# Kernel optimization log

Hardware: AMD Instinct MI355X
Metric: run time of the kernel (lower is better)

The kernel has to match this reference:

```python
import jax, jax.numpy as jnp
import numpy as np

N_HEADS = 16

def setup_inputs() -> dict:
    key = jax.random.key(0)
    k1, k2, k3 = jax.random.split(key, 3)
    B, T, C = 2, 2048, 1024
    x = jax.random.normal(k1, (B, T, C), dtype=jnp.float32)
    W_qkv = jax.random.normal(k2, (3 * C, C), dtype=jnp.float32) * 0.02
    b_qkv = jnp.zeros((3 * C,), dtype=jnp.float32)
    W_proj = jax.random.normal(k3, (C, C), dtype=jnp.float32) * 0.02
    b_proj = jnp.zeros((C,), dtype=jnp.float32)
    return {"x": x, "W_qkv": W_qkv, "b_qkv": b_qkv, "W_proj": W_proj, "b_proj": b_proj}

def reference(x, W_qkv, b_qkv, W_proj, b_proj):
    B, T, C = x.shape
    H = N_HEADS
    hd = C // H
    # fused QKV projection: (B,T,3C)
    qkv = x @ W_qkv.T + b_qkv
    # mirror torch: reshape to (B,T,H,3*hd) then chunk along last dim
    qkv = qkv.reshape(B, T, H, 3 * hd)
    q, k, v = jnp.split(qkv, 3, axis=-1)  # each (B,T,H,hd)
    q = q / jnp.sqrt(jnp.asarray(hd, dtype=q.dtype))
    # scaled dot-product attention, non-causal, full matrix (faithful to source)
    att = jnp.einsum('bihd,bjhd->bhij', q, k)  # (B,H,T,T)
    att = jax.nn.softmax(att, axis=-1)
    out = jnp.einsum('bhij,bjhd->bihd', att, v)  # (B,T,H,hd)
    out = out.reshape(B, T, C)
    return out @ W_proj.T + b_proj
```

## Files before the change

### kernel.cpp

```cpp
#include <hip/hip_runtime.h>


typedef __bf16 bf16x4 __attribute__((ext_vector_type(4)));
typedef __bf16 bf16x8 __attribute__((ext_vector_type(8)));
typedef float  f32x4  __attribute__((ext_vector_type(4)));

#define AS1(p) ((const __attribute__((address_space(1))) void*)(p))
#define AS3(p) ((__attribute__((address_space(3))) void*)(p))

__global__ __launch_bounds__(256)
void cvt_all(const float* __restrict__ a, const float* __restrict__ b,
             const float* __restrict__ c, __bf16* __restrict__ oa,
             __bf16* __restrict__ ob, __bf16* __restrict__ oc,
             int na, int nb, int nc)
{
    const int total = (na + nb + nc) >> 2;
    const int stride = gridDim.x * blockDim.x;
    for (int i4 = blockIdx.x * blockDim.x + threadIdx.x; i4 < total; i4 += stride) {
        int i = i4 << 2;
        const float* src; __bf16* dst;
        if (i < na)               { src = a + i;             dst = oa + i; }
        else if (i < na + nb)     { src = b + (i - na);      dst = ob + (i - na); }
        else                      { src = c + (i - na - nb); dst = oc + (i - na - nb); }
        const float4 v = *(const float4*)src;
        bf16x4 o = { (__bf16)v.x, (__bf16)v.y, (__bf16)v.z, (__bf16)v.w };
        *(bf16x4*)dst = o;
    }
}

__global__ __launch_bounds__(256)
void gemm_qkv(const __bf16* __restrict__ A, const __bf16* __restrict__ W,
              const float* __restrict__ bias, int K,
              __bf16* __restrict__ O0, __bf16* __restrict__ O1,
              __bf16* __restrict__ O2)
{
    __shared__ __bf16 sA[128 * 64];
    __shared__ __bf16 sB[128 * 64];
    const int tid  = threadIdx.x;
    const int w    = tid >> 6, lane = tid & 63;
    const int g    = lane >> 4, r16 = lane & 15;
    const int lin  = blockIdx.y * gridDim.x + blockIdx.x;
    const int per  = (gridDim.x * gridDim.y) >> 3;
    const int nlin = (lin & 7) * per + (lin >> 3);
    const int tM   = (nlin / gridDim.x) * 128, tN = (nlin % gridDim.x) * 128;
    const int wr   = w >> 1, wc = w & 1;
    const int crow = lane >> 3;
    const int ccol = (lane & 7) * 8;

    f32x4 acc[4][4] = {};

    for (int k0 = 0; k0 < K; k0 += 64) {
#pragma unroll
        for (int c = w; c < 16; c += 4) {
            const __bf16* ga = A + (size_t)(tM + c * 8 + crow) * K + k0 + ccol;
            __builtin_amdgcn_global_load_lds(AS1(ga), AS3(&sA[c * 8 * 64]), 16, 0, 0);
            const __bf16* gb = W + (size_t)(tN + c * 8 + crow) * K + k0 + ccol;
            __builtin_amdgcn_global_load_lds(AS1(gb), AS3(&sB[c * 8 * 64]), 16, 0, 0);
        }
        __syncthreads();
#pragma unroll
        for (int kk = 0; kk < 2; ++kk) {
            bf16x8 a[4], b[4];
#pragma unroll
            for (int mf = 0; mf < 4; ++mf)
                a[mf] = *(const bf16x8*)&sA[(wr * 64 + mf * 16 + r16) * 64 + kk * 32 + g * 8];
#pragma unroll
            for (int nf = 0; nf < 4; ++nf)
                b[nf] = *(const bf16x8*)&sB[(wc * 64 + nf * 16 + r16) * 64 + kk * 32 + g * 8];
#pragma unroll
            for (int mf = 0; mf < 4; ++mf)
#pragma unroll
                for (int nf = 0; nf < 4; ++nf)
                    acc[mf][nf] = __builtin_amdgcn_mfma_f32_16x16x32_bf16(
                        a[mf], b[nf], acc[mf][nf], 0, 0, 0);
        }
        __syncthreads();
    }

#pragma unroll
    for (int mf = 0; mf < 4; ++mf) {
#pragma unroll
        for (int nf = 0; nf < 4; ++nf) {
            const int col  = tN + wc * 64 + nf * 16 + r16;
            const int h    = col / 192, j = col % 192;
            const int rowb = tM + wr * 64 + mf * 16 + g * 4;
            const int b    = rowb >> 11, t = rowb & 2047;
            const size_t bh = (size_t)(b * 16 + h);
            const float bs = bias[col];
            if (j >= 128) {
                bf16x4 pk = { (__bf16)(acc[mf][nf][0] + bs), (__bf16)(acc[mf][nf][1] + bs),
                              (__bf16)(acc[mf][nf][2] + bs), (__bf16)(acc[mf][nf][3] + bs) };
                *(bf16x4*)&O2[(bh * 64 + (j - 128)) * 2048 + t] = pk;
            } else if (j < 64) {
#pragma unroll
                for (int reg = 0; reg < 4; ++reg)
                    O0[(bh * 2048 + t + reg) * 64 + j] =
                        (__bf16)((acc[mf][nf][reg] + bs) * 0.18033688011112042f);
            } else {
#pragma unroll
                for (int reg = 0; reg < 4; ++reg)
                    O1[(bh * 2048 + t + reg) * 64 + (j - 64)] =
                        (__bf16)(acc[mf][nf][reg] + bs);
            }
        }
    }
}

__global__ __launch_bounds__(256)
void gemm_proj(const __bf16* __restrict__ A, const __bf16* __restrict__ W,
               const float* __restrict__ bias, int N, int K,
               float* __restrict__ Of)
{
    __shared__ __bf16 sA[128 * 64];
    __shared__ __bf16 sB[64 * 64];
    const int tid  = threadIdx.x;
    const int w    = tid >> 6, lane = tid & 63;
    const int g    = lane >> 4, r16 = lane & 15;
    const int lin  = blockIdx.y * gridDim.x + blockIdx.x;
    const int per  = (gridDim.x * gridDim.y) >> 3;
    const int nlin = (lin & 7) * per + (lin >> 3);
    const int tM   = (nlin / gridDim.x) * 128, tN = (nlin % gridDim.x) * 64;
    const int wr   = w >> 1, wc = w & 1;
    const int crow = lane >> 3;
    const int ccol = (lane & 7) * 8;

    f32x4 acc[4][2] = {};

    for (int k0 = 0; k0 < K; k0 += 64) {
#pragma unroll
        for (int c = w; c < 16; c += 4) {
            const __bf16* ga = A + (size_t)(tM + c * 8 + crow) * K + k0 + ccol;
            __builtin_amdgcn_global_load_lds(AS1(ga), AS3(&sA[c * 8 * 64]), 16, 0, 0);
        }
#pragma unroll
        for (int c = w; c < 8; c += 4) {
            const __bf16* gb = W + (size_t)(tN + c * 8 + crow) * K + k0 + ccol;
            __builtin_amdgcn_global_load_lds(AS1(gb), AS3(&sB[c * 8 * 64]), 16, 0, 0);
        }
        __syncthreads();
#pragma unroll
        for (int kk = 0; kk < 2; ++kk) {
            bf16x8 a[4], b[2];
#pragma unroll
            for (int mf = 0; mf < 4; ++mf)
                a[mf] = *(const bf16x8*)&sA[(wr * 64 + mf * 16 + r16) * 64 + kk * 32 + g * 8];
#pragma unroll
            for (int nf = 0; nf < 2; ++nf)
                b[nf] = *(const bf16x8*)&sB[(wc * 32 + nf * 16 + r16) * 64 + kk * 32 + g * 8];
#pragma unroll
            for (int mf = 0; mf < 4; ++mf)
#pragma unroll
                for (int nf = 0; nf < 2; ++nf)
                    acc[mf][nf] = __builtin_amdgcn_mfma_f32_16x16x32_bf16(
                        a[mf], b[nf], acc[mf][nf], 0, 0, 0);
        }
        __syncthreads();
    }

#pragma unroll
    for (int mf = 0; mf < 4; ++mf)
#pragma unroll
        for (int nf = 0; nf < 2; ++nf) {
            const int col = tN + wc * 32 + nf * 16 + r16;
            const float bs = bias[col];
#pragma unroll
            for (int reg = 0; reg < 4; ++reg) {
                const int row = tM + wr * 64 + mf * 16 + g * 4 + reg;
                Of[(size_t)row * N + col] = acc[mf][nf][reg] + bs;
            }
        }
}

__global__ __launch_bounds__(256, 4)
void attn(const __bf16* __restrict__ Q, const __bf16* __restrict__ K,
          const __bf16* __restrict__ V, __bf16* __restrict__ O)
{
    __shared__ __bf16 sK[2][64 * 64];
    __shared__ __bf16 sV[2][64 * 64];

    const int tid = threadIdx.x;
    const int w   = tid >> 6, lane = tid & 63;
    const int g   = lane >> 4, r16 = lane & 15;
    const int m   = blockIdx.x + (blockIdx.y << 5) + (blockIdx.z << 9);
    const int bh  = (m & 7) + ((m >> 8) << 3);
    const int qb  = (m >> 3) & 31;
    const int q0  = qb * 64 + w * 16;
    const __bf16* Qp = Q + (size_t)bh * 2048 * 64;
    const __bf16* Kp = K + (size_t)bh * 2048 * 64;
    const __bf16* Vp = V + (size_t)bh * 64 * 2048;

    const int srow  = lane >> 3;
    const int scolV = 8 * ((lane & 7) ^ srow);
    const int scolK = 8 * ((lane & 7) ^ ((srow & 3) | ((w & 1) << 2)));
    const int swzK  = ((r16 & 3) | (((r16 >> 2) & 1) << 2)) << 4;
    const int swzV  = (r16 & 7) << 4;

    bf16x8 qa[2];
#pragma unroll
    for (int kk = 0; kk < 2; ++kk)
        qa[kk] = *(const bf16x8*)(Qp + (size_t)(q0 + r16) * 64 + kk * 32 + g * 8);

    bf16x8 ones;
#pragma unroll
    for (int i = 0; i < 8; ++i) ones[i] = (__bf16)1.0f;

    f32x4 o[4] = {};
    f32x4 lsum = {};
    float mrun = 0.f;

    const int row0 = w * 8 + srow;
    const int row1 = 32 + w * 8 + srow;
    const char* kp0 = (const char*)(Kp + (size_t)row0 * 64 + scolK);
    const char* kp1 = (const char*)(Kp + (size_t)row1 * 64 + scolK);
    const char* vp0 = (const char*)(Vp + (size_t)row0 * 2048 + scolV);
    const char* vp1 = (const char*)(Vp + (size_t)row1 * 2048 + scolV);
    const int ldsb0 = w * 1024, ldsb1 = 4096 + w * 1024;

    __builtin_amdgcn_global_load_lds(AS1(kp0), AS3((char*)&sK[0][0] + ldsb0), 16, 0, 0);
    __builtin_amdgcn_global_load_lds(AS1(kp1), AS3((char*)&sK[0][0] + ldsb1), 16, 0, 0);
    __builtin_amdgcn_global_load_lds(AS1(vp0), AS3((char*)&sV[0][0] + ldsb0), 16, 0, 0);
    __builtin_amdgcn_global_load_lds(AS1(vp1), AS3((char*)&sV[0][0] + ldsb1), 16, 0, 0);
    kp0 += 8192; kp1 += 8192; vp0 += 128; vp1 += 128;
    __syncthreads();

    for (int t = 0; t < 32; ++t) {
        const int cur = t & 1;
        if (t < 31) {
            char* const kd = (char*)&sK[cur ^ 1][0];
            char* const vd = (char*)&sV[cur ^ 1][0];
            __builtin_amdgcn_global_load_lds(AS1(kp0), AS3(kd + ldsb0), 16, 0, 0);
            __builtin_amdgcn_global_load_lds(AS1(kp1), AS3(kd + ldsb1), 16, 0, 0);
            __builtin_amdgcn_global_load_lds(AS1(vp0), AS3(vd + ldsb0), 16, 0, 0);
            __builtin_amdgcn_global_load_lds(AS1(vp1), AS3(vd + ldsb1), 16, 0, 0);
            kp0 += 8192; kp1 += 8192; vp0 += 128; vp1 += 128;
        }
        bf16x8 kb[4][2];
#pragma unroll
        for (int nf = 0; nf < 4; ++nf) {
            const int row = ((nf >> 1) << 5) + ((r16 >> 2) << 3) + ((nf & 1) << 2) + (r16 & 3);
#pragma unroll
            for (int kk = 0; kk < 2; ++kk)
                kb[nf][kk] = *(const bf16x8*)((const char*)&sK[cur][0] + row * 128
                                              + ((kk * 64 + g * 16) ^ swzK));
        }
        const f32x4 cinit = { -mrun, -mrun, -mrun, -mrun };
        f32x4 S[4];
        __builtin_amdgcn_s_setprio(1);
#pragma unroll
        for (int nf = 0; nf < 4; ++nf) {
            f32x4 s = __builtin_amdgcn_mfma_f32_16x16x32_bf16(kb[nf][0], qa[0], cinit, 0, 0, 0);
            S[nf]   = __builtin_amdgcn_mfma_f32_16x16x32_bf16(kb[nf][1], qa[1], s, 0, 0, 0);
        }
        __builtin_amdgcn_s_setprio(0);
        float rm = fmaxf(fmaxf(S[0][0], S[0][1]), fmaxf(S[0][2], S[0][3]));
#pragma unroll
        for (int nf = 1; nf < 4; ++nf)
            rm = fmaxf(rm, fmaxf(fmaxf(S[nf][0], S[nf][1]), fmaxf(S[nf][2], S[nf][3])));
        if (!__all(rm <= 8.f)) {
            rm = fmaxf(rm, __shfl_xor(rm, 16));
            rm = fmaxf(rm, __shfl_xor(rm, 32));
            const float delta = fmaxf(rm, 0.f);
            const float al = __builtin_amdgcn_exp2f(-delta);
#pragma unroll
            for (int df = 0; df < 4; ++df)
#pragma unroll
                for (int reg = 0; reg < 4; ++reg) o[df][reg] *= al;
#pragma unroll
            for (int reg = 0; reg < 4; ++reg) lsum[reg] *= al;
            mrun += delta;
#pragma unroll
            for (int nf = 0; nf < 4; ++nf)
#pragma unroll
                for (int reg = 0; reg < 4; ++reg) S[nf][reg] -= delta;
        }
        bf16x8 pb[2];
#pragma unroll
        for (int kk = 0; kk < 2; ++kk) {
            bf16x8 tpk;
            tpk[0] = (__bf16)__builtin_amdgcn_exp2f(S[kk * 2][0]);
            tpk[1] = (__bf16)__builtin_amdgcn_exp2f(S[kk * 2][1]);
            tpk[2] = (__bf16)__builtin_amdgcn_exp2f(S[kk * 2][2]);
            tpk[3] = (__bf16)__builtin_amdgcn_exp2f(S[kk * 2][3]);
            tpk[4] = (__bf16)__builtin_amdgcn_exp2f(S[kk * 2 + 1][0]);
            tpk[5] = (__bf16)__builtin_amdgcn_exp2f(S[kk * 2 + 1][1]);
            tpk[6] = (__bf16)__builtin_amdgcn_exp2f(S[kk * 2 + 1][2]);
            tpk[7] = (__bf16)__builtin_amdgcn_exp2f(S[kk * 2 + 1][3]);
            pb[kk] = tpk;
        }
        __builtin_amdgcn_s_setprio(1);
        lsum = __builtin_amdgcn_mfma_f32_16x16x32_bf16(ones, pb[0], lsum, 0, 0, 0);
        lsum = __builtin_amdgcn_mfma_f32_16x16x32_bf16(ones, pb[1], lsum, 0, 0, 0);
#pragma unroll
        for (int kk = 0; kk < 2; ++kk)
#pragma unroll
            for (int df = 0; df < 4; ++df) {
                const int row = df * 16 + r16;
                bf16x8 vb = *(const bf16x8*)((const char*)&sV[cur][0] + row * 128
                                             + ((kk * 64 + g * 16) ^ swzV));
                o[df] = __builtin_amdgcn_mfma_f32_16x16x32_bf16(vb, pb[kk], o[df], 0, 0, 0);
            }
        __builtin_amdgcn_s_setprio(0);
        __syncthreads();
    }

    const float inv = 1.f / lsum[0];
    const size_t token = (size_t)(bh >> 4) * 2048 + q0 + r16;
#pragma unroll
    for (int df = 0; df < 4; ++df) {
        bf16x4 ov = { (__bf16)(o[df][0] * inv), (__bf16)(o[df][1] * inv),
                      (__bf16)(o[df][2] * inv), (__bf16)(o[df][3] * inv) };
        *(bf16x4*)(O + token * 1024 + (bh & 15) * 64 + df * 16 + g * 4) = ov;
    }
}

extern "C" void kernel_launch(void* const* d_in, const int* in_sizes, int n_in,
                              void* d_out, int out_size, void* d_ws, size_t ws_size,
                              hipStream_t stream)
{
    const float* x     = (const float*)d_in[0];
    const float* Wqkv  = (const float*)d_in[1];
    const float* bqkv  = (const float*)d_in[2];
    const float* Wproj = (const float*)d_in[3];
    const float* bproj = (const float*)d_in[4];
    float* out = (float*)d_out;

    const size_t NX   = (size_t)4096 * 1024;
    const size_t NWQ  = (size_t)3072 * 1024;
    const size_t NWP  = (size_t)1024 * 1024;

    __bf16* xb  = (__bf16*)d_ws;
    __bf16* Wqb = xb  + NX;
    __bf16* Wpb = Wqb + NWQ;
    __bf16* Qs  = Wpb + NWP;
    __bf16* Ks  = Qs  + NX;
    __bf16* Vt  = Ks  + NX;
    __bf16* Os  = Vt  + NX;

    cvt_all<<<dim3(2048), dim3(256), 0, stream>>>(x, Wqkv, Wproj, xb, Wqb, Wpb,
                                                  (int)NX, (int)NWQ, (int)NWP);
    gemm_qkv<<<dim3(24, 32), dim3(256), 0, stream>>>(xb, Wqb, bqkv, 1024, Qs, Ks, Vt);
    attn<<<dim3(32, 16, 2), dim3(256), 0, stream>>>(Qs, Ks, Vt, Os);
    gemm_proj<<<dim3(16, 32), dim3(256), 0, stream>>>(Os, Wpb, bproj, 1024, 1024, out);
}
```

Measured before the change: 119.8 us.

## Software-pipeline QK^T one tile ahead of softmax and PV in attention loop

The attention loop now computes the score tile for the next K block while the current block's softmax and PV MMAs run, with K prefetched two tiles ahead and V one tile ahead. A pending-delta correction subtracts any running-max rescale from the precomputed scores, since they were biased with the old max. This is meant to overlap the exp/softmax VALU work with MFMA work and hide LDS latency. In exchange it costs extra registers for the second score set, which may lower occupancy.

```diff
diff --git a/kernel.cpp b/kernel.cpp
--- a/kernel.cpp
+++ b/kernel.cpp
@@ -206,7 +206,7 @@
 
     f32x4 o[4] = {};
     f32x4 lsum = {};
-    float mrun = 0.f;
+    float mrun = 0.f, pend = 0.f;
 
     const int row0 = w * 8 + srow;
     const int row1 = 32 + w * 8 + srow;
@@ -221,37 +221,72 @@
     __builtin_amdgcn_global_load_lds(AS1(vp0), AS3((char*)&sV[0][0] + ldsb0), 16, 0, 0);
     __builtin_amdgcn_global_load_lds(AS1(vp1), AS3((char*)&sV[0][0] + ldsb1), 16, 0, 0);
     kp0 += 8192; kp1 += 8192; vp0 += 128; vp1 += 128;
+    __builtin_amdgcn_global_load_lds(AS1(kp0), AS3((char*)&sK[1][0] + ldsb0), 16, 0, 0);
+    __builtin_amdgcn_global_load_lds(AS1(kp1), AS3((char*)&sK[1][0] + ldsb1), 16, 0, 0);
+    kp0 += 8192; kp1 += 8192;
     __syncthreads();
 
+    f32x4 S[4];
+    {
+        bf16x8 kb[4][2];
+#pragma unroll
+        for (int nf = 0; nf < 4; ++nf) {
+            const int row = ((nf >> 1) << 5) + ((r16 >> 2) << 3) + ((nf & 1) << 2) + (r16 & 3);
+#pragma unroll
+            for (int kk = 0; kk < 2; ++kk)
+                kb[nf][kk] = *(const bf16x8*)((const char*)&sK[0][0] + row * 128
+                                              + ((kk * 64 + g * 16) ^ swzK));
+        }
+        const f32x4 z = {};
+#pragma unroll
+        for (int nf = 0; nf < 4; ++nf) {
+            f32x4 s = __builtin_amdgcn_mfma_f32_16x16x32_bf16(kb[nf][0], qa[0], z, 0, 0, 0);
+            S[nf]   = __builtin_amdgcn_mfma_f32_16x16x32_bf16(kb[nf][1], qa[1], s, 0, 0, 0);
+        }
+    }
+    __syncthreads();
+
     for (int t = 0; t < 32; ++t) {
-        const int cur = t & 1;
-        if (t < 31) {
-            char* const kd = (char*)&sK[cur ^ 1][0];
-            char* const vd = (char*)&sV[cur ^ 1][0];
+        const int cur = t & 1, nxt = cur ^ 1;
+        if (t < 30) {
+            char* const kd = (char*)&sK[cur][0];
             __builtin_amdgcn_global_load_lds(AS1(kp0), AS3(kd + ldsb0), 16, 0, 0);
             __builtin_amdgcn_global_load_lds(AS1(kp1), AS3(kd + ldsb1), 16, 0, 0);
+            kp0 += 8192; kp1 += 8192;
+        }
+        if (t < 31) {
+            char* const vd = (char*)&sV[nxt][0];
             __builtin_amdgcn_global_load_lds(AS1(vp0), AS3(vd + ldsb0), 16, 0, 0);
             __builtin_amdgcn_global_load_lds(AS1(vp1), AS3(vd + ldsb1), 16, 0, 0);
-            kp0 += 8192; kp1 += 8192; vp0 += 128; vp1 += 128;
-        }
-        bf16x8 kb[4][2];
-#pragma unroll
-        for (int nf = 0; nf < 4; ++nf) {
-            const int row = ((nf >> 1) << 5) + ((r16 >> 2) << 3) + ((nf & 1) << 2) + (r16 & 3);
-#pragma unroll
-            for (int kk = 0; kk < 2; ++kk)
-                kb[nf][kk] = *(const bf16x8*)((const char*)&sK[cur][0] + row * 128
-                                              + ((kk * 64 + g * 16) ^ swzK));
-        }
-        const f32x4 cinit = { -mrun, -mrun, -mrun, -mrun };
-        f32x4 S[4];
-        __builtin_amdgcn_s_setprio(1);
-#pragma unroll
-        for (int nf = 0; nf < 4; ++nf) {
-            f32x4 s = __builtin_amdgcn_mfma_f32_16x16x32_bf16(kb[nf][0], qa[0], cinit, 0, 0, 0);
-            S[nf]   = __builtin_amdgcn_mfma_f32_16x16x32_bf16(kb[nf][1], qa[1], s, 0, 0, 0);
-        }
-        __builtin_amdgcn_s_setprio(0);
+            vp0 += 128; vp1 += 128;
+        }
+        f32x4 Sn[4];
+        if (t < 31) {
+            bf16x8 kb[4][2];
+#pragma unroll
+            for (int nf = 0; nf < 4; ++nf) {
+                const int row = ((nf >> 1) << 5) + ((r16 >> 2) << 3) + ((nf & 1) << 2) + (r16 & 3);
+#pragma unroll
+                for (int kk = 0; kk < 2; ++kk)
+                    kb[nf][kk] = *(const bf16x8*)((const char*)&sK[nxt][0] + row * 128
+                                                  + ((kk * 64 + g * 16) ^ swzK));
+            }
+            const f32x4 cinit = { -mrun, -mrun, -mrun, -mrun };
+            __builtin_amdgcn_s_setprio(1);
+#pragma unroll
+            for (int nf = 0; nf < 4; ++nf) {
+                f32x4 s = __builtin_amdgcn_mfma_f32_16x16x32_bf16(kb[nf][0], qa[0], cinit, 0, 0, 0);
+                Sn[nf]  = __builtin_amdgcn_mfma_f32_16x16x32_bf16(kb[nf][1], qa[1], s, 0, 0, 0);
+            }
+            __builtin_amdgcn_s_setprio(0);
+        }
+        if (__any(pend != 0.f)) {
+#pragma unroll
+            for (int nf = 0; nf < 4; ++nf)
+#pragma unroll
+                for (int reg = 0; reg < 4; ++reg) S[nf][reg] -= pend;
+            pend = 0.f;
+        }
         float rm = fmaxf(fmaxf(S[0][0], S[0][1]), fmaxf(S[0][2], S[0][3]));
 #pragma unroll
         for (int nf = 1; nf < 4; ++nf)
@@ -268,6 +303,7 @@
 #pragma unroll
             for (int reg = 0; reg < 4; ++reg) lsum[reg] *= al;
             mrun += delta;
+            pend = delta;
 #pragma unroll
             for (int nf = 0; nf < 4; ++nf)
 #pragma unroll
@@ -301,6 +337,10 @@
             }
         __builtin_amdgcn_s_setprio(0);
         __syncthreads();
+        if (t < 31) {
+#pragma unroll
+            for (int nf = 0; nf < 4; ++nf) S[nf] = Sn[nf];
+        }
     }
 
     const float inv = 1.f / lsum[0];
```

New measurement: 121.8 us. No clear change (+1.7%).
